# Optimization experiments

Measured on AMD Instinct MI355X. Metric: run time of the kernel, lower is better.

Reference implementation:

```python
import jax, jax.numpy as jnp
import numpy as np

N_HEADS, N_LEVELS, N_POINTS = 8, 4, 4
D_MODEL, UNIT = 384, 128

@jax.custom_vjp
def grl(x):
    # Gradient Reversal Layer: identity forward, -grad backward (lambda_=1)
    return x

def _grl_fwd(x):
    return x, None

def _grl_bwd(res, g):
    return (-g,)

grl.defvjp(_grl_fwd, _grl_bwd)


def ms_deform_attn_core(value, spatial_shapes_np, loc, attn):
    """Multi-scale deformable attention (grid_sample bilinear, zeros padding, align_corners=False).
    value: (N, Len_in, nH, hd)   loc: (N, Lq, nH, nL, nP, 2) normalized [0,1]   attn: (N, Lq, nH, nL, nP)
    """
    N, Lq, nH, nL, nP, _ = loc.shape
    hd = value.shape[-1]
    b = jnp.arange(N).reshape(N, 1, 1, 1)
    h = jnp.arange(nH).reshape(1, 1, nH, 1)
    out = jnp.zeros((N, Lq, nH, hd), dtype=value.dtype)
    start = 0
    for l in range(nL):
        H, W = int(spatial_shapes_np[l, 0]), int(spatial_shapes_np[l, 1])
        v = value[:, start:start + H * W]  # (N, H*W, nH, hd)
        start += H * W
        # align_corners=False pixel coords
        x = loc[:, :, :, l, :, 0] * W - 0.5
        y = loc[:, :, :, l, :, 1] * H - 0.5
        x0f, y0f = jnp.floor(x), jnp.floor(y)
        lx, ly = x - x0f, y - y0f
        x0, y0 = x0f.astype(jnp.int32), y0f.astype(jnp.int32)
        def gather(xi, yi):
            valid = ((xi >= 0) & (xi < W) & (yi >= 0) & (yi < H)).astype(value.dtype)
            flat = jnp.clip(yi, 0, H - 1) * W + jnp.clip(xi, 0, W - 1)  # (N,Lq,nH,nP)
            return v[b, flat, h] * valid[..., None]  # (N,Lq,nH,nP,hd)
        s = (((1 - lx) * (1 - ly))[..., None] * gather(x0, y0)
             + (lx * (1 - ly))[..., None] * gather(x0 + 1, y0)
             + ((1 - lx) * ly)[..., None] * gather(x0, y0 + 1)
             + (lx * ly)[..., None] * gather(x0 + 1, y0 + 1))
        out = out + jnp.sum(s * attn[:, :, :, l, :, None], axis=3)
    return out.reshape(N, Lq, nH * hd)


def setup_inputs() -> dict:
    key = jax.random.key(0)
    ks = jax.random.split(key, 12)
    N, Lq = 2, 5440
    spatial = np.array([[64, 64], [32, 32], [16, 16], [8, 8]], dtype=np.int32)
    sizes = spatial[:, 0] * spatial[:, 1]
    Len_in = int(sizes.sum())  # 5440
    lsi = np.concatenate([[0], np.cumsum(sizes)[:-1]]).astype(np.int32)
    D, U, nH, nL, nP = D_MODEL, UNIT, N_HEADS, N_LEVELS, N_POINTS
    def lin(k, fin, fout):
        return jax.random.normal(k, (fin, fout), jnp.float32) / np.sqrt(fin)
    # faithful grid-init bias for sampling offsets
    thetas = np.arange(nH) * (2.0 * np.pi / nH)
    grid = np.stack([np.cos(thetas), np.sin(thetas)], -1)
    grid = grid / np.abs(grid).max(-1, keepdims=True)
    grid = np.tile(grid.reshape(nH, 1, 1, 2), (1, nL, nP, 1))
    for i in range(nP):
        grid[:, :, i, :] *= (i + 1)
    return {
        "query": jax.random.normal(ks[0], (N, Lq, D), jnp.float32),
        "reference_points": jax.random.uniform(ks[1], (N, Lq, nL, 2), jnp.float32),
        "input_flatten": jax.random.normal(ks[2], (N, Len_in, D), jnp.float32),
        "input_spatial_shapes": jnp.asarray(spatial),
        "input_level_start_index": jnp.asarray(lsi),
        "W_off": 0.01 * jax.random.normal(ks[3], (2 * U, nH * nL * nP * 2), jnp.float32),
        "b_off": jnp.asarray(grid.reshape(-1), dtype=jnp.float32),
        "W_attn": lin(ks[4], 2 * U, nH * nL * nP),
        "b_attn": jnp.zeros((nH * nL * nP,), jnp.float32),
        "W_val": lin(ks[5], 2 * U, 3 * U),
        "b_val": jnp.zeros((3 * U,), jnp.float32),
        "W_out": lin(ks[6], 3 * U, 2 * U),
        "b_out": jnp.zeros((2 * U,), jnp.float32),
        "W_attn_zd": lin(ks[7], 3 * U, nH * nL * nP),
        "b_attn_zd": jnp.zeros((nH * nL * nP,), jnp.float32),
        "W_val_zd": lin(ks[8], D, D),
        "b_val_zd": jnp.zeros((D,), jnp.float32),
        "W_out_zd": lin(ks[9], D, U),
        "b_out_zd": jnp.zeros((U,), jnp.float32),
    }


def reference(query, reference_points, input_flatten, input_spatial_shapes, input_level_start_index,
              W_off, b_off, W_attn, b_attn, W_val, b_val, W_out, b_out,
              W_attn_zd, b_attn_zd, W_val_zd, b_val_zd, W_out_zd, b_out_zd):
    N, Lq, _ = query.shape
    nH, nL, nP, U = N_HEADS, N_LEVELS, N_POINTS, UNIT
    ss = np.asarray(input_spatial_shapes)  # static level shapes
    sample_query = query[..., :2 * U]
    off = (sample_query @ W_off + b_off).reshape(N, Lq, nH, nL, nP, 2)
    # offset normalizer = [W_l, H_l] per level
    norm = jnp.asarray(np.stack([ss[:, 1], ss[:, 0]], -1), dtype=query.dtype)
    loc = reference_points[:, :, None, :, None, :] + off / norm[None, None, None, :, None, :]
    # top (content) path
    top_val = (input_flatten[..., :2 * U] @ W_val + b_val).reshape(N, -1, nH, 3 * U // nH)
    aw = jax.nn.softmax((sample_query @ W_attn + b_attn).reshape(N, Lq, nH, nL * nP), -1)
    aw = aw.reshape(N, Lq, nH, nL, nP)
    top_out = ms_deform_attn_core(top_val, ss, loc, aw) @ W_out + b_out
    # bottom (domain) path with gradient reversal on content slice
    bot_val_in = jnp.concatenate([grl(input_flatten[..., :2 * U]), input_flatten[..., 2 * U:]], -1)
    bot_val = (bot_val_in @ W_val_zd + b_val_zd).reshape(N, -1, nH, D_MODEL // nH)
    bot_query = jnp.concatenate([grl(query[..., :2 * U]), query[..., 2 * U:]], -1)
    aw_zd = jax.nn.softmax((bot_query @ W_attn_zd + b_attn_zd).reshape(N, Lq, nH, nL * nP), -1)
    aw_zd = aw_zd.reshape(N, Lq, nH, nL, nP)
    bot_out = ms_deform_attn_core(bot_val, ss, loc, aw_zd) @ W_out_zd + b_out_zd
    return jnp.concatenate([top_out, bot_out], -1)
```

## Files before the change

### kernel.cpp

```cpp
#include <hip/hip_runtime.h>
#include <hip/hip_bf16.h>
#include <math.h>

#define DM   384
#define U2   256
#define HD   48

typedef __attribute__((ext_vector_type(8))) short short8;
typedef __attribute__((ext_vector_type(4))) float floatx4;

static __device__ __forceinline__ unsigned short f2bfbits(float f) {
    __hip_bfloat16 h = __float2bfloat16(f);
    return *reinterpret_cast<unsigned short*>(&h);
}
static __device__ __forceinline__ unsigned pack2(float x, float y) {
    return (unsigned)f2bfbits(x) | ((unsigned)f2bfbits(y) << 16);
}
static __device__ __forceinline__ float bflo(unsigned u) { return __uint_as_float(u << 16); }
static __device__ __forceinline__ float bfhi(unsigned u) { return __uint_as_float(u & 0xffff0000u); }

struct PrepParams {
    const float* wsrc[7]; __hip_bfloat16* wdst[7];
    int K[7], N[7], off[8];
    int total;
};
__global__ __launch_bounds__(256) void prep_kernel(PrepParams d) {
    const int iw = blockIdx.x * 256 + threadIdx.x;
    if (iw >= d.total) return;
    int s = 0;
#pragma unroll
    for (int i = 1; i < 7; ++i) if (iw >= d.off[i]) s = i;
    const int r = iw - d.off[s];
    const int k = r / d.N[s], n = r - k * d.N[s];
    d.wdst[s][(size_t)n * d.K[s] + k] = __float2bfloat16(d.wsrc[s][r]);
}

struct Seg {
    const void* A; int lda; int aty;
    const __hip_bfloat16* Bt; int ldbt;
    const float* bias; void* C; int ldc; int K; int omode;
};
struct SegParams { Seg seg[5]; int ystart[5]; int nseg; };

__global__ __launch_bounds__(256) void gemm_seg_kernel(SegParams p) {
    __shared__ __hip_bfloat16 As[128 * 40];
    __shared__ __hip_bfloat16 Bs[128 * 40];

    const int yb = blockIdx.y;
    int s = 0;
#pragma unroll
    for (int i = 1; i < 5; ++i) if (i < p.nseg && yb >= p.ystart[i]) s = i;
    Seg sg;
    switch (s) {
        case 0: sg = p.seg[0]; break;
        case 1: sg = p.seg[1]; break;
        case 2: sg = p.seg[2]; break;
        case 3: sg = p.seg[3]; break;
        default: sg = p.seg[4]; break;
    }
    const int by = yb - p.ystart[s];

    const int t    = threadIdx.x;
    const int bm   = blockIdx.x * 128;
    const int bn   = by * 128;
    const int w    = t >> 6, lane = t & 63;
    const int wm   = (w >> 1) * 64, wn = (w & 1) * 64;
    const int quad = lane >> 4, lm = lane & 15;

    const int r0 = t >> 2, kc = (t & 3) * 8;

    floatx4 acc[4][4] = {};

    for (int k0 = 0; k0 < sg.K; k0 += 32) {
#pragma unroll
        for (int g = 0; g < 2; ++g) {
            const int row = r0 + 64 * g;
            if (sg.aty) {
                *(short8*)&As[row * 40 + kc] =
                    *(const short8*)((const __hip_bfloat16*)sg.A +
                        (size_t)(bm + row) * sg.lda + k0 + kc);
            } else {
                const float* src = (const float*)sg.A +
                    (size_t)(bm + row) * sg.lda + k0 + kc;
                const float4 f0 = *(const float4*)(src + 0);
                const float4 f1 = *(const float4*)(src + 4);
                uint4 u;
                u.x = pack2(f0.x, f0.y); u.y = pack2(f0.z, f0.w);
                u.z = pack2(f1.x, f1.y); u.w = pack2(f1.z, f1.w);
                *(uint4*)&As[row * 40 + kc] = u;
            }
            *(short8*)&Bs[row * 40 + kc] =
                *(const short8*)&sg.Bt[(size_t)(bn + row) * sg.ldbt + k0 + kc];
        }
        __syncthreads();

        short8 af[4], bf[4];
#pragma unroll
        for (int i = 0; i < 4; ++i)
            af[i] = *(const short8*)&As[(wm + i * 16 + lm) * 40 + quad * 8];
#pragma unroll
        for (int j = 0; j < 4; ++j)
            bf[j] = *(const short8*)&Bs[(wn + j * 16 + lm) * 40 + quad * 8];
#pragma unroll
        for (int i = 0; i < 4; ++i)
#pragma unroll
            for (int j = 0; j < 4; ++j)
                acc[i][j] = __builtin_amdgcn_mfma_f32_16x16x32_bf16(
                    af[i], bf[j], acc[i][j], 0, 0, 0);
        __syncthreads();
    }

#pragma unroll
    for (int i = 0; i < 4; ++i)
#pragma unroll
        for (int reg = 0; reg < 4; ++reg) {
            const int row = bm + wm + i * 16 + quad * 4 + reg;
#pragma unroll
            for (int j = 0; j < 4; ++j) {
                const int col = bn + wn + j * 16 + lm;
                const float v = acc[i][j][reg] + sg.bias[col];
                if (sg.omode == 0) {
                    ((float*)sg.C)[(size_t)row * sg.ldc + col] = v;
                } else if (sg.omode == 1) {
                    ((__hip_bfloat16*)sg.C)[(size_t)row * sg.ldc + col] = __float2bfloat16(v);
                } else {
                    const int h = col / 48;
                    const size_t idx = (size_t)row * 768 + h * 96 +
                                       ((sg.omode == 3) ? 48 : 0) + (col - h * 48);
                    ((__hip_bfloat16*)sg.C)[idx] = __float2bfloat16(v);
                }
            }
        }
}

#define SPP 524

__global__ __launch_bounds__(192) void sampler_kernel(
    const float* __restrict__ off_buf,
    const float* __restrict__ logit_top,
    const float* __restrict__ logit_bot,
    const float* __restrict__ ref_pts,
    const int*   __restrict__ ss,
    const int*   __restrict__ lsi,
    const __hip_bfloat16* __restrict__ vcomb,
    __hip_bfloat16* __restrict__ core_top,
    __hip_bfloat16* __restrict__ core_bot,
    int Lq, int LenIn)
{
    __shared__ float    sA[2][128];
    __shared__ unsigned sP[2][SPP];
    __shared__ float4   sRed[96][2];

    const int bid = blockIdx.x;
    const int t   = threadIdx.x;

    float gw[4];
    int   gp[4];

    if (t < 128) {
        const int e = t;
        const int n = bid / Lq;
        const int l = (e >> 2) & 3;
        const float2 offv = *(const float2*)&off_buf[(size_t)bid * 256 + 2 * e];
        const float rx = ref_pts[(size_t)(bid * 4 + l) * 2 + 0];
        const float ry = ref_pts[(size_t)(bid * 4 + l) * 2 + 1];
        const int H = ss[2 * l], W = ss[2 * l + 1];
        const int start = lsi[l];

        const float x = (rx + offv.x / (float)W) * (float)W - 0.5f;
        const float y = (ry + offv.y / (float)H) * (float)H - 0.5f;
        const float x0f = floorf(x), y0f = floorf(y);
        const float lx = x - x0f, ly = y - y0f;
        const int ix0 = (int)x0f, iy0 = (int)y0f;
        const int ix1 = ix0 + 1,  iy1 = iy0 + 1;

        const float vx0 = (ix0 >= 0 && ix0 < W) ? 1.f : 0.f;
        const float vx1 = (ix1 >= 0 && ix1 < W) ? 1.f : 0.f;
        const float vy0 = (iy0 >= 0 && iy0 < H) ? 1.f : 0.f;
        const float vy1 = (iy1 >= 0 && iy1 < H) ? 1.f : 0.f;
        const int cx0 = min(max(ix0, 0), W - 1);
        const int cx1 = min(max(ix1, 0), W - 1);
        const int cy0 = min(max(iy0, 0), H - 1);
        const int cy1 = min(max(iy1, 0), H - 1);
        const int base = bid / Lq * LenIn + start;
        (void)n;

        gp[0] = base + cy0 * W + cx0;
        gp[1] = base + cy0 * W + cx1;
        gp[2] = base + cy1 * W + cx0;
        gp[3] = base + cy1 * W + cx1;
        gw[0] = (1.f - lx) * (1.f - ly) * vx0 * vy0;
        gw[1] = lx * (1.f - ly) * vx1 * vy0;
        gw[2] = (1.f - lx) * ly * vx0 * vy1;
        gw[3] = lx * ly * vx1 * vy1;
    }

    if (t < 16) {
        const int br = t >> 3;
        const int h  = t & 7;
        const float* L = (br ? logit_bot : logit_top) + (size_t)bid * 128 + h * 16;
        float lg[16];
        *(float4*)&lg[0]  = *(const float4*)&L[0];
        *(float4*)&lg[4]  = *(const float4*)&L[4];
        *(float4*)&lg[8]  = *(const float4*)&L[8];
        *(float4*)&lg[12] = *(const float4*)&L[12];
        float m = -1e30f;
#pragma unroll
        for (int j = 0; j < 16; ++j) m = fmaxf(m, lg[j]);
        float ex[16], sum = 0.f;
#pragma unroll
        for (int j = 0; j < 16; ++j) { ex[j] = expf(lg[j] - m); sum += ex[j]; }
        const float inv = 1.f / sum;
#pragma unroll
        for (int j = 0; j < 16; ++j) sA[br][h * 16 + j] = ex[j] * inv;
    }
    __syncthreads();

    if (t < 128) {
        const int e = t;
        const int pidx = 4 * e + (e >> 4);
#pragma unroll
        for (int br = 0; br < 2; ++br) {
            const float a = sA[br][e];
#pragma unroll
            for (int k = 0; k < 4; ++k) {
                sP[br][pidx + k] =
                    ((unsigned)f2bfbits(gw[k] * a) << 16) | (unsigned)gp[k];
            }
        }
    }
    __syncthreads();

    const int half = t / 96;
    const int u    = t - half * 96;
    const int g    = u / 6;
    const int m    = u - g * 6;
    const int br   = g & 1;
    const int h    = g >> 1;

    const unsigned* P = sP[br];
    const char* vb = (const char*)vcomb + h * 192 + br * 96 + m * 16;

    float a0 = 0.f, a1 = 0.f, a2 = 0.f, a3 = 0.f;
    float a4 = 0.f, a5 = 0.f, a6 = 0.f, a7 = 0.f;
    const int lp0 = half * 8;
#pragma unroll
    for (int lp = 0; lp < 8; ++lp) {
        const int ib = 65 * h + 4 * (lp0 + lp);
#pragma unroll
        for (int k = 0; k < 4; ++k) {
            const unsigned uu = P[ib + k];
            const float wv = __uint_as_float(uu & 0xffff0000u);
            const unsigned pt = uu & 0x3fffu;
            const uint4 v = *(const uint4*)(vb + pt * 1536u);
            a0 = fmaf(wv, bflo(v.x), a0);
            a1 = fmaf(wv, bfhi(v.x), a1);
            a2 = fmaf(wv, bflo(v.y), a2);
            a3 = fmaf(wv, bfhi(v.y), a3);
            a4 = fmaf(wv, bflo(v.z), a4);
            a5 = fmaf(wv, bfhi(v.z), a5);
            a6 = fmaf(wv, bflo(v.w), a6);
            a7 = fmaf(wv, bfhi(v.w), a7);
        }
    }

    if (half) {
        float4 p0; p0.x = a0; p0.y = a1; p0.z = a2; p0.w = a3;
        float4 p1; p1.x = a4; p1.y = a5; p1.z = a6; p1.w = a7;
        sRed[u][0] = p0;
        sRed[u][1] = p1;
    }
    __syncthreads();
    if (!half) {
        const float4 p0 = sRed[u][0];
        const float4 p1 = sRed[u][1];
        uint4 o;
        o.x = pack2(a0 + p0.x, a1 + p0.y);
        o.y = pack2(a2 + p0.z, a3 + p0.w);
        o.z = pack2(a4 + p1.x, a5 + p1.y);
        o.w = pack2(a6 + p1.z, a7 + p1.w);
        __hip_bfloat16* dst = br ? core_bot : core_top;
        *(uint4*)&dst[(size_t)bid * DM + h * HD + m * 8] = o;
    }
}

extern "C" void kernel_launch(void* const* d_in, const int* in_sizes, int n_in,
                              void* d_out, int out_size, void* d_ws, size_t ws_size,
                              hipStream_t stream) {
    const float* query   = (const float*)d_in[0];
    const float* refpts  = (const float*)d_in[1];
    const float* flat    = (const float*)d_in[2];
    const int*   ss      = (const int*)d_in[3];
    const int*   lsi     = (const int*)d_in[4];
    const float* W_off   = (const float*)d_in[5];
    const float* b_off   = (const float*)d_in[6];
    const float* W_attn  = (const float*)d_in[7];
    const float* b_attn  = (const float*)d_in[8];
    const float* W_val   = (const float*)d_in[9];
    const float* b_val   = (const float*)d_in[10];
    const float* W_out   = (const float*)d_in[11];
    const float* b_out   = (const float*)d_in[12];
    const float* W_attn_zd = (const float*)d_in[13];
    const float* b_attn_zd = (const float*)d_in[14];
    const float* W_val_zd  = (const float*)d_in[15];
    const float* b_val_zd  = (const float*)d_in[16];
    const float* W_out_zd  = (const float*)d_in[17];
    const float* b_out_zd  = (const float*)d_in[18];

    const int Lq    = in_sizes[0] / (2 * DM);
    const int LenIn = in_sizes[2] / (2 * DM);
    const int M  = 2 * Lq;
    const int Mv = 2 * LenIn;

    float* out = (float*)d_out;

    float* ws      = (float*)d_ws;
    float* off_buf = ws;
    float* lt      = off_buf + (size_t)M * 256;
    float* lb      = lt + (size_t)M * 128;
    __hip_bfloat16* vcomb = (__hip_bfloat16*)(lb + (size_t)M * 128);
    __hip_bfloat16* ct    = vcomb + (size_t)Mv * 768;
    __hip_bfloat16* cb    = ct + (size_t)M * 384;
    __hip_bfloat16* wtb   = cb + (size_t)M * 384;

    PrepParams pp;
    const float* srcs[7] = {W_attn, W_attn_zd, W_val, W_val_zd, W_out, W_out_zd, W_off};
    const int Ks[7] = {256, 384, 256, 384, 384, 384, 256};
    const int Ns[7] = {128, 128, 384, 384, 256, 128, 256};
    __hip_bfloat16* dsts[7];
    int off = 0;
    for (int i = 0; i < 7; ++i) {
        pp.wsrc[i] = srcs[i]; pp.K[i] = Ks[i]; pp.N[i] = Ns[i];
        pp.off[i] = off;
        dsts[i] = wtb + off;
        pp.wdst[i] = dsts[i];
        off += Ks[i] * Ns[i];
    }
    pp.off[7] = off;
    pp.total = off;

    const dim3 blk(256);
    const int mg = M / 128;

    prep_kernel<<<dim3((pp.total + 255) / 256), blk, 0, stream>>>(pp);

    {
        SegParams p;
        p.seg[0] = { query, DM, 0, dsts[6], 256, b_off,     off_buf, 256, 256, 0 };
        p.seg[1] = { query, DM, 0, dsts[0], 256, b_attn,    lt,      128, 256, 0 };
        p.seg[2] = { query, DM, 0, dsts[1], 384, b_attn_zd, lb,      128, 384, 0 };
        p.seg[3] = { flat,  DM, 0, dsts[2], 256, b_val,     vcomb,   0,   256, 2 };
        p.seg[4] = { flat,  DM, 0, dsts[3], 384, b_val_zd,  vcomb,   0,   384, 3 };
        p.ystart[0] = 0; p.ystart[1] = 2; p.ystart[2] = 3;
        p.ystart[3] = 4; p.ystart[4] = 7;
        p.nseg = 5;
        gemm_seg_kernel<<<dim3(mg, 10), blk, 0, stream>>>(p);
    }

    sampler_kernel<<<dim3(M), dim3(192), 0, stream>>>(
        off_buf, lt, lb, refpts, ss, lsi, vcomb, ct, cb, Lq, LenIn);

    {
        SegParams p;
        p.seg[0] = { ct, DM, 1, dsts[4], 384, b_out,    out,      DM, 384, 0 };
        p.seg[1] = { cb, DM, 1, dsts[5], 384, b_out_zd, out + U2, DM, 384, 0 };
        p.ystart[0] = 0; p.ystart[1] = 2;
        p.nseg = 2;
        gemm_seg_kernel<<<dim3(mg, 3), blk, 0, stream>>>(p);
    }
}
```

Baseline: 255.9 us.

## Shrink GEMM tiles to 64x64 and prefetch next K-slice into registers

The segmented GEMM kernel now uses 64x64 output tiles with each wave computing 32x32, which doubles the grid in both dimensions for more blocks across CUs. It also adds register prefetching: the next K-slice of A and B is loaded from global memory while the current slice is multiplied out of shared memory. The aim is better CU occupancy for these small GEMMs (M around 10880) and hiding global load latency. In exchange, each tile has less data reuse, so global traffic per FLOP goes up.

```diff
diff --git a/kernel.cpp b/kernel.cpp
--- a/kernel.cpp
+++ b/kernel.cpp
@@ -43,8 +43,8 @@
 struct SegParams { Seg seg[5]; int ystart[5]; int nseg; };
 
 __global__ __launch_bounds__(256) void gemm_seg_kernel(SegParams p) {
-    __shared__ __hip_bfloat16 As[128 * 40];
-    __shared__ __hip_bfloat16 Bs[128 * 40];
+    __shared__ __hip_bfloat16 As[64 * 40];
+    __shared__ __hip_bfloat16 Bs[64 * 40];
 
     const int yb = blockIdx.y;
     int s = 0;
@@ -61,62 +61,76 @@
     const int by = yb - p.ystart[s];
 
     const int t    = threadIdx.x;
-    const int bm   = blockIdx.x * 128;
-    const int bn   = by * 128;
+    const int bm   = blockIdx.x * 64;
+    const int bn   = by * 64;
     const int w    = t >> 6, lane = t & 63;
-    const int wm   = (w >> 1) * 64, wn = (w & 1) * 64;
+    const int wm   = (w >> 1) * 32, wn = (w & 1) * 32;
     const int quad = lane >> 4, lm = lane & 15;
 
     const int r0 = t >> 2, kc = (t & 3) * 8;
 
-    floatx4 acc[4][4] = {};
-
+    float4 fa0, fa1;
+    short8 abf;
+    short8 bbf;
+
+    const bool atyb = (sg.aty != 0);
+
+#define LOAD_REGS(K0)                                                          \
+    do {                                                                       \
+        if (atyb) {                                                            \
+            abf = *(const short8*)((const __hip_bfloat16*)sg.A +               \
+                (size_t)(bm + r0) * sg.lda + (K0) + kc);                       \
+        } else {                                                               \
+            const float* _src = (const float*)sg.A +                           \
+                (size_t)(bm + r0) * sg.lda + (K0) + kc;                        \
+            fa0 = *(const float4*)_src;                                        \
+            fa1 = *(const float4*)(_src + 4);                                  \
+        }                                                                      \
+        bbf = *(const short8*)&sg.Bt[(size_t)(bn + r0) * sg.ldbt + (K0) + kc]; \
+    } while (0)
+
+    floatx4 acc[2][2] = {};
+
+    LOAD_REGS(0);
     for (int k0 = 0; k0 < sg.K; k0 += 32) {
-#pragma unroll
-        for (int g = 0; g < 2; ++g) {
-            const int row = r0 + 64 * g;
-            if (sg.aty) {
-                *(short8*)&As[row * 40 + kc] =
-                    *(const short8*)((const __hip_bfloat16*)sg.A +
-                        (size_t)(bm + row) * sg.lda + k0 + kc);
-            } else {
-                const float* src = (const float*)sg.A +
-                    (size_t)(bm + row) * sg.lda + k0 + kc;
-                const float4 f0 = *(const float4*)(src + 0);
-                const float4 f1 = *(const float4*)(src + 4);
-                uint4 u;
-                u.x = pack2(f0.x, f0.y); u.y = pack2(f0.z, f0.w);
-                u.z = pack2(f1.x, f1.y); u.w = pack2(f1.z, f1.w);
-                *(uint4*)&As[row * 40 + kc] = u;
-            }
-            *(short8*)&Bs[row * 40 + kc] =
-                *(const short8*)&sg.Bt[(size_t)(bn + row) * sg.ldbt + k0 + kc];
+        if (atyb) {
+            *(short8*)&As[r0 * 40 + kc] = abf;
+        } else {
+            uint4 u;
+            u.x = pack2(fa0.x, fa0.y); u.y = pack2(fa0.z, fa0.w);
+            u.z = pack2(fa1.x, fa1.y); u.w = pack2(fa1.z, fa1.w);
+            *(uint4*)&As[r0 * 40 + kc] = u;
         }
+        *(short8*)&Bs[r0 * 40 + kc] = bbf;
         __syncthreads();
 
-        short8 af[4], bf[4];
-#pragma unroll
-        for (int i = 0; i < 4; ++i)
+        const int kn = k0 + 32;
+        if (kn < sg.K) LOAD_REGS(kn);
+
+        short8 af[2], bf[2];
+#pragma unroll
+        for (int i = 0; i < 2; ++i)
             af[i] = *(const short8*)&As[(wm + i * 16 + lm) * 40 + quad * 8];
 #pragma unroll
-        for (int j = 0; j < 4; ++j)
+        for (int j = 0; j < 2; ++j)
             bf[j] = *(const short8*)&Bs[(wn + j * 16 + lm) * 40 + quad * 8];
 #pragma unroll
-        for (int i = 0; i < 4; ++i)
-#pragma unroll
-            for (int j = 0; j < 4; ++j)
+        for (int i = 0; i < 2; ++i)
+#pragma unroll
+            for (int j = 0; j < 2; ++j)
                 acc[i][j] = __builtin_amdgcn_mfma_f32_16x16x32_bf16(
                     af[i], bf[j], acc[i][j], 0, 0, 0);
         __syncthreads();
     }
-
-#pragma unroll
-    for (int i = 0; i < 4; ++i)
+#undef LOAD_REGS
+
+#pragma unroll
+    for (int i = 0; i < 2; ++i)
 #pragma unroll
         for (int reg = 0; reg < 4; ++reg) {
             const int row = bm + wm + i * 16 + quad * 4 + reg;
 #pragma unroll
-            for (int j = 0; j < 4; ++j) {
+            for (int j = 0; j < 2; ++j) {
                 const int col = bn + wn + j * 16 + lm;
                 const float v = acc[i][j][reg] + sg.bias[col];
                 if (sg.omode == 0) {
@@ -159,7 +173,6 @@
 
     if (t < 128) {
         const int e = t;
-        const int n = bid / Lq;
         const int l = (e >> 2) & 3;
         const float2 offv = *(const float2*)&off_buf[(size_t)bid * 256 + 2 * e];
         const float rx = ref_pts[(size_t)(bid * 4 + l) * 2 + 0];
@@ -183,7 +196,6 @@
         const int cy0 = min(max(iy0, 0), H - 1);
         const int cy1 = min(max(iy1, 0), H - 1);
         const int base = bid / Lq * LenIn + start;
-        (void)n;
 
         gp[0] = base + cy0 * W + cx0;
         gp[1] = base + cy0 * W + cx1;
@@ -340,7 +352,7 @@
     pp.total = off;
 
     const dim3 blk(256);
-    const int mg = M / 128;
+    const int mg = M / 64;
 
     prep_kernel<<<dim3((pp.total + 255) / 256), blk, 0, stream>>>(pp);
 
@@ -351,10 +363,10 @@
         p.seg[2] = { query, DM, 0, dsts[1], 384, b_attn_zd, lb,      128, 384, 0 };
         p.seg[3] = { flat,  DM, 0, dsts[2], 256, b_val,     vcomb,   0,   256, 2 };
         p.seg[4] = { flat,  DM, 0, dsts[3], 384, b_val_zd,  vcomb,   0,   384, 3 };
-        p.ystart[0] = 0; p.ystart[1] = 2; p.ystart[2] = 3;
-        p.ystart[3] = 4; p.ystart[4] = 7;
+        p.ystart[0] = 0; p.ystart[1] = 4; p.ystart[2] = 6;
+        p.ystart[3] = 8; p.ystart[4] = 14;
         p.nseg = 5;
-        gemm_seg_kernel<<<dim3(mg, 10), blk, 0, stream>>>(p);
+        gemm_seg_kernel<<<dim3(mg, 20), blk, 0, stream>>>(p);
     }
 
     sampler_kernel<<<dim3(M), dim3(192), 0, stream>>>(
@@ -364,8 +376,8 @@
         SegParams p;
         p.seg[0] = { ct, DM, 1, dsts[4], 384, b_out,    out,      DM, 384, 0 };
         p.seg[1] = { cb, DM, 1, dsts[5], 384, b_out_zd, out + U2, DM, 384, 0 };
-        p.ystart[0] = 0; p.ystart[1] = 2;
+        p.ystart[0] = 0; p.ystart[1] = 4;
         p.nseg = 2;
-        gemm_seg_kernel<<<dim3(mg, 3), blk, 0, stream>>>(p);
-    }
-}
+        gemm_seg_kernel<<<dim3(mg, 6), blk, 0, stream>>>(p);
+    }
+}
```

After: 229.9 us. 10.1% less time.
